# Kernel optimization log

Hardware: AMD Instinct MI355X
Metric: run time of the kernel (lower is better)

Reference implementation:

```python
import jax, jax.numpy as jnp
import numpy as np

D_MODEL = 1024
N_HEADS = 32
HEAD_DIM = D_MODEL // N_HEADS
EPS = 1e-5


def setup_inputs() -> dict:
    key = jax.random.key(0)
    ks = jax.random.split(key, 6)
    B, S = 2, 2048
    scale = 1.0 / np.sqrt(D_MODEL)
    return {
        "x": jax.random.normal(ks[0], (B, S, D_MODEL), dtype=jnp.float32),
        "Wqkv_w": jax.random.normal(ks[1], (3 * D_MODEL, D_MODEL), dtype=jnp.float32) * scale,
        "Wqkv_b": jax.random.normal(ks[2], (3 * D_MODEL,), dtype=jnp.float32) * 0.01,
        "gn_w": jnp.ones((D_MODEL,), dtype=jnp.float32),
        "gn_b": jnp.zeros((D_MODEL,), dtype=jnp.float32),
        "out_w": jax.random.normal(ks[3], (D_MODEL, D_MODEL), dtype=jnp.float32) * scale,
        "out_b": jax.random.normal(ks[4], (D_MODEL,), dtype=jnp.float32) * 0.01,
    }


def reference(x, Wqkv_w, Wqkv_b, gn_w, gn_b, out_w, out_b):
    B, S, Dm = x.shape
    H, Dh = N_HEADS, HEAD_DIM
    # QKV projection
    qkv = x @ Wqkv_w.T + Wqkv_b                      # [B,S,3*Dm]
    qkv = qkv.reshape(B, S, 3, H, Dh)
    q, k, v = qkv[:, :, 0], qkv[:, :, 1], qkv[:, :, 2]  # each [B,S,H,Dh]
    # Linear (softmax-free) attention; dropout p=0 -> identity
    a = jnp.einsum('bthd,bshd->bhts', q, k)          # [B,H,S,S]
    ctx = jnp.einsum('bhts,bshd->bthd', a, v)        # [B,S,H,Dh]
    # GroupNorm(num_groups=H, num_channels=Dm) on transposed (B, Dm, S):
    # normalizes jointly over (Dh channels, S positions) per (batch, group)
    g = ctx.transpose(0, 2, 3, 1)                    # [B,H,Dh,S]
    mean = g.mean(axis=(2, 3), keepdims=True)
    var = ((g - mean) ** 2).mean(axis=(2, 3), keepdims=True)
    gh = (g - mean) * jax.lax.rsqrt(var + EPS)
    gh = gh * gn_w.reshape(H, Dh, 1) + gn_b.reshape(H, Dh, 1)
    ctx = gh.transpose(0, 3, 1, 2).reshape(B, S, Dm)  # back to [B,S,Dm]
    return ctx @ out_w.T + out_b
```

## Files before the change

### kernel.cpp

```cpp
#include <hip/hip_runtime.h>
#include <hip/hip_bf16.h>
#include <stdint.h>

typedef unsigned short ushort_t;
typedef __attribute__((ext_vector_type(4))) float f32x4;
typedef __attribute__((ext_vector_type(8))) short short8;

#define SS 2048
#define ROWS 4096
#define EPS 1e-5f

__device__ __forceinline__ unsigned short f2bf(float f) {
  unsigned int u = __float_as_uint(f);
  u += 0x7FFF + ((u >> 16) & 1);
  return (unsigned short)(u >> 16);
}
__device__ __forceinline__ float bf2f(short s) {
  return __uint_as_float(((unsigned int)(unsigned short)s) << 16);
}

__global__ __launch_bounds__(256) void f2b_kernel(const float* __restrict__ in,
                                                  ushort_t* __restrict__ out, int n4) {
  int stride = gridDim.x * blockDim.x;
  for (int i = blockIdx.x * blockDim.x + threadIdx.x; i < n4; i += stride) {
    float4 v = reinterpret_cast<const float4*>(in)[i];
    ushort4 o;
    o.x = f2bf(v.x); o.y = f2bf(v.y); o.z = f2bf(v.z); o.w = f2bf(v.w);
    reinterpret_cast<ushort4*>(out)[i] = o;
  }
}

#define GLDS16(g, l)                                                        \
  __builtin_amdgcn_global_load_lds((__attribute__((address_space(1))) void*)(g), \
                                   (__attribute__((address_space(3))) void*)(l), 16, 0, 0)

template <int OUTBF16>
__global__ __launch_bounds__(256) void gemm_bt(const ushort_t* __restrict__ A,
                                               const ushort_t* __restrict__ B,
                                               const float* __restrict__ bias,
                                               void* __restrict__ Cv,
                                               int M, int N, int K, int dualB) {
  __shared__ __align__(16) ushort_t As[128 * 32];
  __shared__ __align__(16) ushort_t Bs[128 * 32];
  const int tid = threadIdx.x;
  const int wave = tid >> 6, lane = tid & 63;
  const int bm = blockIdx.x * 128, bn = blockIdx.y * 128;
  if (dualB && bm >= 2048) { B += (size_t)N * K; bias += N; }
  const int wr = (wave >> 1) * 64, wc = (wave & 1) * 64;

  f32x4 acc[4][4] = {};

  const int srow = lane >> 2;
  const int scol = (lane & 3) * 8;
  const ushort_t* ga0 = A + (size_t)(bm + wave * 16 + srow) * K + scol;
  const ushort_t* ga1 = A + (size_t)(bm + 64 + wave * 16 + srow) * K + scol;
  const ushort_t* gb0 = B + (size_t)(bn + wave * 16 + srow) * K + scol;
  const ushort_t* gb1 = B + (size_t)(bn + 64 + wave * 16 + srow) * K + scol;
  ushort_t* la0 = &As[wave * 512];
  ushort_t* la1 = &As[(wave + 4) * 512];
  ushort_t* lb0 = &Bs[wave * 512];
  ushort_t* lb1 = &Bs[(wave + 4) * 512];

  const int aoff = (wr + (lane & 15)) * 32 + (lane >> 4) * 8;
  const int boff = (wc + (lane & 15)) * 32 + (lane >> 4) * 8;

  for (int k0 = 0; k0 < K; k0 += 32) {
    if (k0) __syncthreads();
    GLDS16(ga0 + k0, la0);
    GLDS16(ga1 + k0, la1);
    GLDS16(gb0 + k0, lb0);
    GLDS16(gb1 + k0, lb1);
    __syncthreads();

    short8 av[4], bv[4];
#pragma unroll
    for (int m = 0; m < 4; ++m)
      av[m] = *reinterpret_cast<const short8*>(&As[aoff + m * 16 * 32]);
#pragma unroll
    for (int n = 0; n < 4; ++n)
      bv[n] = *reinterpret_cast<const short8*>(&Bs[boff + n * 16 * 32]);
#pragma unroll
    for (int m = 0; m < 4; ++m)
#pragma unroll
      for (int n = 0; n < 4; ++n)
        acc[m][n] = __builtin_amdgcn_mfma_f32_16x16x32_bf16(av[m], bv[n], acc[m][n], 0, 0, 0);
  }

  const int crow0 = bm + wr + (lane >> 4) * 4;
  const int ccol0 = bn + wc + (lane & 15);
#pragma unroll
  for (int m = 0; m < 4; ++m)
#pragma unroll
    for (int n = 0; n < 4; ++n) {
      const int col = ccol0 + n * 16;
      const float bb = bias[col];
#pragma unroll
      for (int j = 0; j < 4; ++j) {
        const int row = crow0 + m * 16 + j;
        const float val = acc[m][n][j] + bb;
        if constexpr (OUTBF16) {
          ((ushort_t*)Cv)[(size_t)row * N + col] = f2bf(val);
        } else {
          ((float*)Cv)[(size_t)row * N + col] = val;
        }
      }
    }
}

__global__ __launch_bounds__(256) void kv_partial(const ushort_t* __restrict__ qkvb,
                                                  float* __restrict__ KVp) {
  __shared__ float kt[64 * 32];
  __shared__ float vt[64 * 32];
  const int blk = blockIdx.x;
  const int bh = blk >> 5;
  const int ch = blk & 31;
  const int b = bh >> 5, h = bh & 31;
  const int tid = threadIdx.x;
  const int r = tid >> 2, cg = (tid & 3) * 8;
  const ushort_t* kp = qkvb + (size_t)(b * SS + ch * 64 + r) * 3072 + 1024 + h * 32 + cg;
  const short8 k8 = *(const short8*)kp;
  const short8 v8 = *(const short8*)(kp + 1024);
#pragma unroll
  for (int i = 0; i < 8; ++i) {
    kt[r * 32 + cg + i] = bf2f(k8[i]);
    vt[r * 32 + cg + i] = bf2f(v8[i]);
  }
  __syncthreads();
  const int d = tid & 31, eg = tid >> 5;
  float acc[4] = {0.f, 0.f, 0.f, 0.f};
#pragma unroll 8
  for (int ss = 0; ss < 64; ++ss) {
    const float vv = vt[ss * 32 + d];
#pragma unroll
    for (int i = 0; i < 4; ++i)
      acc[i] += kt[ss * 32 + eg * 4 + i] * vv;
  }
  float* o = KVp + ((size_t)bh * 32 + ch) * 1024 + (eg * 4) * 32 + d;
#pragma unroll
  for (int i = 0; i < 4; ++i) o[i * 32] = acc[i];
}

__global__ __launch_bounds__(256) void kv_reduce(const float* __restrict__ KVp,
                                                 float* __restrict__ KV) {
  const int bh = blockIdx.x;
  const int tid = threadIdx.x;
  const float* base = KVp + (size_t)bh * 32768 + tid * 4;
  float4 s = make_float4(0.f, 0.f, 0.f, 0.f);
  for (int c = 0; c < 32; ++c) {
    const float4 v = *(const float4*)(base + c * 1024);
    s.x += v.x; s.y += v.y; s.z += v.z; s.w += v.w;
  }
  *(float4*)&KV[(size_t)bh * 1024 + tid * 4] = s;
}

__global__ __launch_bounds__(256) void ctx_kernel(const ushort_t* __restrict__ qkvb,
                                                  const float* __restrict__ KV,
                                                  ushort_t* __restrict__ ctxb,
                                                  float2* __restrict__ partials) {
  __shared__ float kvs[1024];
  __shared__ float red[8];
  const int blk = blockIdx.x;
  const int bh = blk >> 3, tt = blk & 7;
  const int b = bh >> 5, h = bh & 31;
  const int tid = threadIdx.x;
  for (int i = tid; i < 1024; i += 256) kvs[i] = KV[(size_t)bh * 1024 + i];
  __syncthreads();
  const int t = tt * 256 + tid;
  const ushort_t* qrow = qkvb + ((size_t)(b * SS + t)) * 3072 + h * 32;
  float q[32];
#pragma unroll
  for (int g = 0; g < 4; ++g) {
    const short8 qv = *(const short8*)(qrow + g * 8);
#pragma unroll
    for (int i = 0; i < 8; ++i) q[g * 8 + i] = bf2f(qv[i]);
  }
  float o[32];
#pragma unroll
  for (int d = 0; d < 32; ++d) o[d] = 0.f;
#pragma unroll
  for (int e = 0; e < 32; ++e) {
    const float qe = q[e];
    const float* kr = &kvs[e * 32];
#pragma unroll
    for (int d = 0; d < 32; ++d) o[d] += qe * kr[d];
  }
  float sum = 0.f, sq = 0.f;
#pragma unroll
  for (int d = 0; d < 32; ++d) { sum += o[d]; sq += o[d] * o[d]; }
  ushort_t* crow = ctxb + ((size_t)(b * SS + t)) * 1024 + h * 32;
#pragma unroll
  for (int g = 0; g < 4; ++g) {
    short8 ov;
#pragma unroll
    for (int i = 0; i < 8; ++i) ov[i] = (short)f2bf(o[g * 8 + i]);
    *(short8*)(crow + g * 8) = ov;
  }
#pragma unroll
  for (int off = 32; off > 0; off >>= 1) {
    sum += __shfl_down(sum, off);
    sq  += __shfl_down(sq, off);
  }
  const int wave = tid >> 6, lane = tid & 63;
  if (lane == 0) { red[wave * 2] = sum; red[wave * 2 + 1] = sq; }
  __syncthreads();
  if (tid == 0) {
    const float s = red[0] + red[2] + red[4] + red[6];
    const float q2 = red[1] + red[3] + red[5] + red[7];
    partials[blk] = make_float2(s, q2);
  }
}

__global__ void stats_kernel(const float2* __restrict__ partials,
                             float2* __restrict__ stats) {
  const int bh = threadIdx.x;
  float s = 0.f, q = 0.f;
  for (int i = 0; i < 8; ++i) { const float2 p = partials[bh * 8 + i]; s += p.x; q += p.y; }
  const float mean = s * (1.f / 65536.f);
  const float var = q * (1.f / 65536.f) - mean * mean;
  stats[bh] = make_float2(mean, rsqrtf(var + EPS));
}

__global__ __launch_bounds__(256) void fold_kernel(const float* __restrict__ W2,
                                                   const float* __restrict__ b2,
                                                   const float* __restrict__ gw,
                                                   const float* __restrict__ gb,
                                                   const float2* __restrict__ stats,
                                                   ushort_t* __restrict__ W2s,
                                                   float* __restrict__ bias2) {
  __shared__ float sS[1024], sT[1024];
  const int b = blockIdx.y;
  const int tid = threadIdx.x;
  {
    const int c0 = tid * 4;
    const float2 st = stats[b * 32 + (c0 >> 5)];
    const float4 w = *(const float4*)&gw[c0];
    const float4 g = *(const float4*)&gb[c0];
    sS[c0]     = st.y * w.x;  sT[c0]     = g.x - st.x * st.y * w.x;
    sS[c0 + 1] = st.y * w.y;  sT[c0 + 1] = g.y - st.x * st.y * w.y;
    sS[c0 + 2] = st.y * w.z;  sT[c0 + 2] = g.z - st.x * st.y * w.z;
    sS[c0 + 3] = st.y * w.w;  sT[c0 + 3] = g.w - st.x * st.y * w.w;
  }
  __syncthreads();
  const int row = blockIdx.x * 16 + (tid >> 4);
  const int l16 = tid & 15;
  float part = 0.f;
  for (int k = 0; k < 16; ++k) {
    const int c = k * 64 + l16 * 4;
    const float4 w2v = *(const float4*)&W2[(size_t)row * 1024 + c];
    ushort4 o;
    o.x = f2bf(w2v.x * sS[c]);
    o.y = f2bf(w2v.y * sS[c + 1]);
    o.z = f2bf(w2v.z * sS[c + 2]);
    o.w = f2bf(w2v.w * sS[c + 3]);
    *(ushort4*)&W2s[(size_t)b * 1048576 + (size_t)row * 1024 + c] = o;
    part += w2v.x * sT[c] + w2v.y * sT[c + 1] + w2v.z * sT[c + 2] + w2v.w * sT[c + 3];
  }
#pragma unroll
  for (int off = 8; off > 0; off >>= 1) part += __shfl_down(part, off, 16);
  if (l16 == 0) bias2[b * 1024 + row] = b2[row] + part;
}

extern "C" void kernel_launch(void* const* d_in, const int* in_sizes, int n_in,
                              void* d_out, int out_size, void* d_ws, size_t ws_size,
                              hipStream_t stream) {
  const float* x  = (const float*)d_in[0];
  const float* w1 = (const float*)d_in[1];
  const float* b1 = (const float*)d_in[2];
  const float* gw = (const float*)d_in[3];
  const float* gb = (const float*)d_in[4];
  const float* w2 = (const float*)d_in[5];
  const float* b2 = (const float*)d_in[6];
  float* out = (float*)d_out;

  char* ws = (char*)d_ws;
  ushort_t* Xb    = (ushort_t*)(ws);
  float*    KVp   = (float*)(ws);
  ushort_t* W1b   = (ushort_t*)(ws + 8388608);
  ushort_t* qkvb  = (ushort_t*)(ws + 16777216);
  ushort_t* ctxb  = (ushort_t*)(ws + 41943040);
  ushort_t* W2s   = (ushort_t*)(ws + 50331648);
  float*    bias2 = (float*)(ws + 54525952);
  float*    KV    = (float*)(ws + 54534144);
  float2*   partials = (float2*)(ws + 54796288);
  float2*   stats    = (float2*)(ws + 54800384);

  f2b_kernel<<<2048, 256, 0, stream>>>(x,  Xb,  ROWS * 1024 / 4);
  f2b_kernel<<<2048, 256, 0, stream>>>(w1, W1b, 3072 * 1024 / 4);
  gemm_bt<1><<<dim3(32, 24), 256, 0, stream>>>(Xb, W1b, b1, qkvb, ROWS, 3072, 1024, 0);
  kv_partial<<<2048, 256, 0, stream>>>(qkvb, KVp);
  kv_reduce<<<64, 256, 0, stream>>>(KVp, KV);
  ctx_kernel<<<512, 256, 0, stream>>>(qkvb, KV, ctxb, partials);
  stats_kernel<<<1, 64, 0, stream>>>(partials, stats);
  fold_kernel<<<dim3(64, 2), 256, 0, stream>>>(w2, b2, gw, gb, stats, W2s, bias2);
  gemm_bt<0><<<dim3(32, 8), 256, 0, stream>>>(ctxb, W2s, bias2, out, ROWS, 1024, 1024, 1);
}
```

Before: 102.8 us.

## Add 4-stage pipelined QKV GEMM and fuse conversion and stats launches

Replaces the QKV projection GEMM with a new 512-thread, 256x192-tile kernel. It uses a 4-deep LDS ring buffer fed by async global-to-LDS loads, explicit vmcnt waits and MFMA priority hints, so memory traffic overlaps with matrix math. It also merges the two fp32-to-bf16 conversion launches into one kernel, and folds the GroupNorm stats reduction into the fold kernel to drop a launch. The trade-offs are heavier LDS use, a hand-counted waitcnt schedule that is fragile if load counts change, and redundant stats computation in every fold block.

```diff
diff --git a/kernel.cpp b/kernel.cpp
--- a/kernel.cpp
+++ b/kernel.cpp
@@ -19,20 +19,130 @@
   return __uint_as_float(((unsigned int)(unsigned short)s) << 16);
 }
 
-__global__ __launch_bounds__(256) void f2b_kernel(const float* __restrict__ in,
-                                                  ushort_t* __restrict__ out, int n4) {
-  int stride = gridDim.x * blockDim.x;
-  for (int i = blockIdx.x * blockDim.x + threadIdx.x; i < n4; i += stride) {
-    float4 v = reinterpret_cast<const float4*>(in)[i];
-    ushort4 o;
-    o.x = f2bf(v.x); o.y = f2bf(v.y); o.z = f2bf(v.z); o.w = f2bf(v.w);
-    reinterpret_cast<ushort4*>(out)[i] = o;
-  }
-}
-
 #define GLDS16(g, l)                                                        \
   __builtin_amdgcn_global_load_lds((__attribute__((address_space(1))) void*)(g), \
                                    (__attribute__((address_space(3))) void*)(l), 16, 0, 0)
+
+__global__ __launch_bounds__(256) void f2b2_kernel(const float* __restrict__ a,
+                                                   ushort_t* __restrict__ oa, int n4a,
+                                                   const float* __restrict__ b,
+                                                   ushort_t* __restrict__ ob, int n4b) {
+  const int stride = gridDim.x * blockDim.x;
+  const int total = n4a + n4b;
+  for (int i = blockIdx.x * blockDim.x + threadIdx.x; i < total; i += stride) {
+    const float4 v = (i < n4a) ? reinterpret_cast<const float4*>(a)[i]
+                               : reinterpret_cast<const float4*>(b)[i - n4a];
+    ushort4 o;
+    o.x = f2bf(v.x); o.y = f2bf(v.y); o.z = f2bf(v.z); o.w = f2bf(v.w);
+    if (i < n4a) reinterpret_cast<ushort4*>(oa)[i] = o;
+    else         reinterpret_cast<ushort4*>(ob)[i - n4a] = o;
+  }
+}
+
+#define MF(d, va, vb) d = __builtin_amdgcn_mfma_f32_16x16x32_bf16(va, vb, d, 0, 0, 0)
+#define LD8(p) (*reinterpret_cast<const short8*>(p))
+
+__global__ __launch_bounds__(512, 2) void gemm1_pipe(const ushort_t* __restrict__ A,
+                                                     const ushort_t* __restrict__ B,
+                                                     const float* __restrict__ bias,
+                                                     ushort_t* __restrict__ C) {
+  __shared__ __align__(16) ushort_t lds[4 * 14336];
+  const int tid = threadIdx.x;
+  const int wid = tid >> 6, lane = tid & 63;
+  const int bm = blockIdx.x * 256, bn = blockIdx.y * 192;
+  const int wm = wid >> 2, wn = wid & 3;
+
+  const int srow = lane >> 2;
+  const int scol = ((lane & 3) ^ ((lane >> 3) & 3)) * 8;
+  const int widb = (wid < 6) ? wid : 0;
+  const ushort_t* gA0 = A + (size_t)(bm + wid * 16 + srow) * 1024 + scol;
+  const ushort_t* gA1 = A + (size_t)(bm + (8 + wid) * 16 + srow) * 1024 + scol;
+  const ushort_t* gB0 = B + (size_t)(bn + widb * 16 + srow) * 1024 + scol;
+  const ushort_t* gB1 = B + (size_t)(bn + (6 + widb) * 16 + srow) * 1024 + scol;
+
+  const int lf = lane & 15, kf = lane >> 4;
+  const int flip = ((lane >> 1) & 3) << 4;
+  const int aBase = (((wm * 128 + lf) * 64 + kf * 16) ^ flip) >> 1;
+  const int bBase = ((((wn * 48 + lf) * 64 + kf * 16) ^ flip) >> 1) + 8192;
+
+  f32x4 acc[8][3] = {};
+
+#define STAGE_A(t)                                                           \
+  { ushort_t* d = lds + (((t) & 3) * 14336);                                 \
+    GLDS16(gA0 + (t) * 32, d + wid * 512);                                   \
+    GLDS16(gA1 + (t) * 32, d + (8 + wid) * 512); }
+#define STAGE_B(t)                                                           \
+  if (wid < 6) { ushort_t* d = lds + (((t) & 3) * 14336) + 8192;             \
+    GLDS16(gB0 + (t) * 32, d + wid * 512);                                   \
+    GLDS16(gB1 + (t) * 32, d + (6 + wid) * 512); }
+
+  STAGE_A(0) STAGE_B(0)
+  STAGE_A(1) STAGE_B(1)
+  STAGE_A(2) STAGE_B(2)
+  if (wid < 6) { asm volatile("s_waitcnt vmcnt(8)" ::: "memory"); }
+  else         { asm volatile("s_waitcnt vmcnt(4)" ::: "memory"); }
+  __builtin_amdgcn_s_barrier();
+  __builtin_amdgcn_sched_barrier(0);
+
+#define K_TILE(t, DO_STAGE, VM6, VM2)                                        \
+  { const ushort_t* Lb = lds + (((t) & 3) * 14336);                          \
+    short8 bv0 = LD8(Lb + bBase);                                            \
+    short8 bv1 = LD8(Lb + bBase + 512);                                      \
+    short8 bv2 = LD8(Lb + bBase + 1024);                                     \
+    short8 a0 = LD8(Lb + aBase);                                             \
+    short8 a1 = LD8(Lb + aBase + 512);                                       \
+    short8 a2 = LD8(Lb + aBase + 1024);                                      \
+    short8 a3 = LD8(Lb + aBase + 1536);                                      \
+    if (DO_STAGE) STAGE_A((t) + 3)                                           \
+    __builtin_amdgcn_s_setprio(1);                                           \
+    MF(acc[0][0], a0, bv0); MF(acc[1][0], a1, bv0);                          \
+    MF(acc[0][1], a0, bv1); MF(acc[1][1], a1, bv1);                          \
+    MF(acc[0][2], a0, bv2); MF(acc[1][2], a1, bv2);                          \
+    MF(acc[2][0], a2, bv0); MF(acc[3][0], a3, bv0);                          \
+    MF(acc[2][1], a2, bv1); MF(acc[3][1], a3, bv1);                          \
+    MF(acc[2][2], a2, bv2); MF(acc[3][2], a3, bv2);                          \
+    __builtin_amdgcn_s_setprio(0);                                           \
+    a0 = LD8(Lb + aBase + 2048);                                             \
+    a1 = LD8(Lb + aBase + 2560);                                             \
+    a2 = LD8(Lb + aBase + 3072);                                             \
+    a3 = LD8(Lb + aBase + 3584);                                             \
+    if (DO_STAGE) STAGE_B((t) + 3)                                           \
+    __builtin_amdgcn_s_setprio(1);                                           \
+    MF(acc[4][0], a0, bv0); MF(acc[5][0], a1, bv0);                          \
+    MF(acc[4][1], a0, bv1); MF(acc[5][1], a1, bv1);                          \
+    MF(acc[4][2], a0, bv2); MF(acc[5][2], a1, bv2);                          \
+    MF(acc[6][0], a2, bv0); MF(acc[7][0], a3, bv0);                          \
+    MF(acc[6][1], a2, bv1); MF(acc[7][1], a3, bv1);                          \
+    MF(acc[6][2], a2, bv2); MF(acc[7][2], a3, bv2);                          \
+    __builtin_amdgcn_s_setprio(0);                                           \
+    __builtin_amdgcn_sched_barrier(0);                                       \
+    if (wid < 6) { asm volatile("s_waitcnt vmcnt(" #VM6 ")" ::: "memory"); } \
+    else         { asm volatile("s_waitcnt vmcnt(" #VM2 ")" ::: "memory"); } \
+    __builtin_amdgcn_s_barrier();                                            \
+    __builtin_amdgcn_sched_barrier(0); }
+
+#pragma unroll 1
+  for (int t = 0; t < 29; ++t) K_TILE(t, 1, 8, 4)
+  K_TILE(29, 0, 4, 2)
+  K_TILE(30, 0, 0, 0)
+  K_TILE(31, 0, 0, 0)
+
+  const int crow = bm + wm * 128 + (lane >> 4) * 4;
+  const int ccol = bn + wn * 48 + (lane & 15);
+#pragma unroll
+  for (int m = 0; m < 8; ++m)
+#pragma unroll
+    for (int n = 0; n < 3; ++n) {
+      const int col = ccol + n * 16;
+      const float bb = bias[col];
+#pragma unroll
+      for (int j = 0; j < 4; ++j)
+        C[(size_t)(crow + m * 16 + j) * 3072 + col] = f2bf(acc[m][n][j] + bb);
+    }
+#undef K_TILE
+#undef STAGE_A
+#undef STAGE_B
+}
 
 template <int OUTBF16>
 __global__ __launch_bounds__(256) void gemm_bt(const ushort_t* __restrict__ A,
@@ -210,35 +320,37 @@
   }
 }
 
-__global__ void stats_kernel(const float2* __restrict__ partials,
-                             float2* __restrict__ stats) {
-  const int bh = threadIdx.x;
-  float s = 0.f, q = 0.f;
-  for (int i = 0; i < 8; ++i) { const float2 p = partials[bh * 8 + i]; s += p.x; q += p.y; }
-  const float mean = s * (1.f / 65536.f);
-  const float var = q * (1.f / 65536.f) - mean * mean;
-  stats[bh] = make_float2(mean, rsqrtf(var + EPS));
-}
-
 __global__ __launch_bounds__(256) void fold_kernel(const float* __restrict__ W2,
                                                    const float* __restrict__ b2,
                                                    const float* __restrict__ gw,
                                                    const float* __restrict__ gb,
-                                                   const float2* __restrict__ stats,
+                                                   const float2* __restrict__ partials,
                                                    ushort_t* __restrict__ W2s,
                                                    float* __restrict__ bias2) {
   __shared__ float sS[1024], sT[1024];
+  __shared__ float sMean[32], sRstd[32];
   const int b = blockIdx.y;
   const int tid = threadIdx.x;
+  if (tid < 32) {
+    float s = 0.f, q = 0.f;
+    for (int i = 0; i < 8; ++i) {
+      const float2 p = partials[(b * 32 + tid) * 8 + i];
+      s += p.x; q += p.y;
+    }
+    const float mean = s * (1.f / 65536.f);
+    const float var = q * (1.f / 65536.f) - mean * mean;
+    sMean[tid] = mean; sRstd[tid] = rsqrtf(var + EPS);
+  }
+  __syncthreads();
   {
     const int c0 = tid * 4;
-    const float2 st = stats[b * 32 + (c0 >> 5)];
+    const float mean = sMean[c0 >> 5], rstd = sRstd[c0 >> 5];
     const float4 w = *(const float4*)&gw[c0];
     const float4 g = *(const float4*)&gb[c0];
-    sS[c0]     = st.y * w.x;  sT[c0]     = g.x - st.x * st.y * w.x;
-    sS[c0 + 1] = st.y * w.y;  sT[c0 + 1] = g.y - st.x * st.y * w.y;
-    sS[c0 + 2] = st.y * w.z;  sT[c0 + 2] = g.z - st.x * st.y * w.z;
-    sS[c0 + 3] = st.y * w.w;  sT[c0 + 3] = g.w - st.x * st.y * w.w;
+    sS[c0]     = rstd * w.x;  sT[c0]     = g.x - mean * rstd * w.x;
+    sS[c0 + 1] = rstd * w.y;  sT[c0 + 1] = g.y - mean * rstd * w.y;
+    sS[c0 + 2] = rstd * w.z;  sT[c0 + 2] = g.z - mean * rstd * w.z;
+    sS[c0 + 3] = rstd * w.w;  sT[c0 + 3] = g.w - mean * rstd * w.w;
   }
   __syncthreads();
   const int row = blockIdx.x * 16 + (tid >> 4);
@@ -282,15 +394,12 @@
   float*    bias2 = (float*)(ws + 54525952);
   float*    KV    = (float*)(ws + 54534144);
   float2*   partials = (float2*)(ws + 54796288);
-  float2*   stats    = (float2*)(ws + 54800384);
-
-  f2b_kernel<<<2048, 256, 0, stream>>>(x,  Xb,  ROWS * 1024 / 4);
-  f2b_kernel<<<2048, 256, 0, stream>>>(w1, W1b, 3072 * 1024 / 4);
-  gemm_bt<1><<<dim3(32, 24), 256, 0, stream>>>(Xb, W1b, b1, qkvb, ROWS, 3072, 1024, 0);
+
+  f2b2_kernel<<<2048, 256, 0, stream>>>(x, Xb, ROWS * 1024 / 4, w1, W1b, 3072 * 1024 / 4);
+  gemm1_pipe<<<dim3(16, 16), 512, 0, stream>>>(Xb, W1b, b1, qkvb);
   kv_partial<<<2048, 256, 0, stream>>>(qkvb, KVp);
   kv_reduce<<<64, 256, 0, stream>>>(KVp, KV);
   ctx_kernel<<<512, 256, 0, stream>>>(qkvb, KV, ctxb, partials);
-  stats_kernel<<<1, 64, 0, stream>>>(partials, stats);
-  fold_kernel<<<dim3(64, 2), 256, 0, stream>>>(w2, b2, gw, gb, stats, W2s, bias2);
+  fold_kernel<<<dim3(64, 2), 256, 0, stream>>>(w2, b2, gw, gb, partials, W2s, bias2);
   gemm_bt<0><<<dim3(32, 8), 256, 0, stream>>>(ctxb, W2s, bias2, out, ROWS, 1024, 1024, 1);
 }
```

Result: faster. 95.36 us (-7.2%).
